# Kernel optimization log

Measured on AMD Instinct MI355X. Metric: run time of the kernel, lower is better.

The kernel has to match this reference:

```python
import jax, jax.numpy as jnp
import numpy as np

IN_FEATURES = 4096
OUT_FEATURES = 11008
GROUP_SIZE = 128


def setup_inputs() -> dict:
    key = jax.random.key(0)
    k_x, k_w, k_s, k_z, k_b = jax.random.split(key, 5)
    x = jax.random.normal(k_x, (8, IN_FEATURES), dtype=jnp.float32)
    # packed INT4 weights: two 4-bit values per byte, stored in int32 (0..255)
    weight_q = jax.random.randint(k_w, (OUT_FEATURES, IN_FEATURES // 2), 0, 256, dtype=jnp.int32)
    num_groups = IN_FEATURES // GROUP_SIZE  # 32
    scales = jax.random.uniform(k_s, (OUT_FEATURES, num_groups), dtype=jnp.float32) * 0.01 + 1e-4
    zeros = jax.random.normal(k_z, (OUT_FEATURES, num_groups), dtype=jnp.float32) * 0.05
    bias = jax.random.normal(k_b, (OUT_FEATURES,), dtype=jnp.float32) * 0.02
    return {"x": x, "weight_q": weight_q, "scales": scales, "zeros": zeros, "bias": bias}


def _dequantize(weight_q, scales, zeros):
    # unpack INT4: low nibble first, then high nibble (matches torch stack order)
    low = weight_q & 15
    high = (weight_q >> 4) & 15
    q = jnp.stack([low, high], axis=-1).reshape(OUT_FEATURES, -1)  # [out, in]
    q = q.astype(scales.dtype)
    num_groups = scales.shape[1]
    q = q[:, : num_groups * GROUP_SIZE].reshape(OUT_FEATURES, num_groups, GROUP_SIZE)
    w = q * scales[:, :, None] + zeros[:, :, None]
    return w.reshape(OUT_FEATURES, -1)[:, :IN_FEATURES]


def reference(x, weight_q, scales, zeros, bias):
    w = _dequantize(weight_q, scales, zeros)            # [out, in]
    return x.astype(w.dtype) @ w.T + bias               # [B, out]
```

## Files before the change

kernel.cpp:

```cpp
#include <hip/hip_runtime.h>

typedef _Float16 f16;
typedef __attribute__((ext_vector_type(2))) _Float16 f16x2;
typedef __attribute__((ext_vector_type(8))) _Float16 f16x8;
typedef __attribute__((ext_vector_type(4))) float f32x4;
typedef __attribute__((ext_vector_type(4))) unsigned u32x4;

constexpr int IN_F  = 4096;
constexpr int OUT_F = 11008;
constexpr int NGRP  = 32;

__device__ __forceinline__ unsigned dq2(unsigned q, f16x2 sp, f16x2 zp) {
    unsigned t = (((q << 12) | q) & 0x000F000Fu) | 0x64006400u;
    f16x2 u = __builtin_bit_cast(f16x2, t);
    u = u - (f16x2){(_Float16)1024.0f, (_Float16)1024.0f};
    u = u * sp + zp;
    return __builtin_bit_cast(unsigned, u);
}

__device__ __forceinline__ f16x2 bcast(float v) {
    _Float16 h = (_Float16)v;
    return (f16x2){h, h};
}

__global__ __launch_bounds__(256, 4)
void qlin_kernel(const int* __restrict__ wq,
                 const float* __restrict__ scales,
                 const float* __restrict__ zeros,
                 const float* __restrict__ bias,
                 const float* __restrict__ xf,
                 float* __restrict__ out)
{
    __shared__ unsigned char wlds[2][16][1024];
    __shared__ f32x4 red[4][64];

    const int tid  = threadIdx.x;
    const int wv   = tid >> 6;
    const int lane = tid & 63;
    const int col  = lane & 15;
    const int kg   = lane >> 4;
    const int o0   = blockIdx.x * 16;
    const int orow = o0 + col;
    const bool mvalid = (col < 8);

    f16x2 sp[8], zp[8];
    #pragma unroll
    for (int s = 0; s < 8; ++s) {
        sp[s] = bcast(scales[(size_t)orow * NGRP + s * 4 + wv]);
        zp[s] = bcast(zeros [(size_t)orow * NGRP + s * 4 + wv]);
    }

    const char* wtile = (const char*)wq + (size_t)o0 * 8192;

    auto stage = [&](int sl, int bufi) {
        #pragma unroll
        for (int c = 0; c < 4; ++c) {
            const int r = 4 * wv + c;
            const char* src = wtile + (size_t)r * 8192 + sl * 1024
                              + ((lane * 16) ^ ((r & 7) << 4));
            __builtin_amdgcn_global_load_lds(
                (const __attribute__((address_space(1))) void*)src,
                (__attribute__((address_space(3))) void*)&wlds[bufi][r][0],
                16, 0, 0);
        }
    };

    stage(0, 0);
    stage(1, 1);

    const float* xfcol = xf + (size_t)col * IN_F;
    const unsigned swz = (unsigned)((col & 7) << 4);

    f32x4 acc = {0.f, 0.f, 0.f, 0.f};

    #pragma unroll
    for (int s = 0; s < 8; ++s) {
        if (s < 7) asm volatile("s_waitcnt vmcnt(4)" ::: "memory");
        else       asm volatile("s_waitcnt vmcnt(0)" ::: "memory");
        __builtin_amdgcn_s_barrier();
        asm volatile("" ::: "memory");

        const f16x2 s2 = sp[s], z2 = zp[s];
        #pragma unroll
        for (int t = 0; t < 4; ++t) {
            const int k = s * 512 + wv * 128 + t * 32 + kg * 8;
            f16x8 af = (f16x8){0,0,0,0,0,0,0,0};
            if (mvalid) {
                float4 a0 = *(const float4*)(xfcol + k);
                float4 a1 = *(const float4*)(xfcol + k + 4);
                af = (f16x8){(f16)a0.x,(f16)a0.y,(f16)a0.z,(f16)a0.w,
                             (f16)a1.x,(f16)a1.y,(f16)a1.z,(f16)a1.w};
            }
            const unsigned off = ((unsigned)(wv * 256 + t * 64 + kg * 16)) ^ swz;
            const int4 q = *(const int4*)&wlds[s & 1][col][off];
            u32x4 bw = {dq2((unsigned)q.x, s2, z2),
                        dq2((unsigned)q.y, s2, z2),
                        dq2((unsigned)q.z, s2, z2),
                        dq2((unsigned)q.w, s2, z2)};
            f16x8 bfr = __builtin_bit_cast(f16x8, bw);
            acc = __builtin_amdgcn_mfma_f32_16x16x32_f16(af, bfr, acc, 0, 0, 0);
        }

        asm volatile("" ::: "memory");
        __builtin_amdgcn_s_barrier();
        if (s < 6) stage(s + 2, s & 1);
    }

    red[wv][lane] = acc;
    __syncthreads();

    if (tid < 64) {
        f32x4 ssum = red[0][tid];
        #pragma unroll
        for (int w = 1; w < 4; ++w) ssum += red[w][tid];
        const int n = tid & 15;
        const float bb = bias[o0 + n];
        const int mbase = (tid >> 4) * 4;
        if (mbase < 8) {
            #pragma unroll
            for (int i = 0; i < 4; ++i)
                out[(size_t)(mbase + i) * OUT_F + o0 + n] = ssum[i] + bb;
        }
    }
}

extern "C" void kernel_launch(void* const* d_in, const int* in_sizes, int n_in,
                              void* d_out, int out_size, void* d_ws, size_t ws_size,
                              hipStream_t stream) {
    const float* x  = (const float*)d_in[0];
    const int*   wq = (const int*)d_in[1];
    const float* sc = (const float*)d_in[2];
    const float* zr = (const float*)d_in[3];
    const float* bs = (const float*)d_in[4];
    float* out = (float*)d_out;
    (void)d_ws; (void)ws_size; (void)in_sizes; (void)n_in;

    qlin_kernel<<<OUT_F / 16, 256, 0, stream>>>(wq, sc, zr, bs, x, out);
}
```

Baseline: 31.70 us.

## Split K across four blocks with workspace partials and a separate reduce kernel

New measurement: 27.67 us. 12.7% less time.

```diff
diff --git a/kernel.cpp b/kernel.cpp
--- a/kernel.cpp
+++ b/kernel.cpp
@@ -9,6 +9,8 @@
 constexpr int IN_F  = 4096;
 constexpr int OUT_F = 11008;
 constexpr int NGRP  = 32;
+constexpr int NTILE = OUT_F / 16;
+constexpr int PLANE = OUT_F * 8;
 
 __device__ __forceinline__ unsigned dq2(unsigned q, f16x2 sp, f16x2 zp) {
     unsigned t = (((q << 12) | q) & 0x000F000Fu) | 0x64006400u;
@@ -21,6 +23,115 @@
 __device__ __forceinline__ f16x2 bcast(float v) {
     _Float16 h = (_Float16)v;
     return (f16x2){h, h};
+}
+
+__global__ __launch_bounds__(256, 4)
+void qlin_partial(const int* __restrict__ wq,
+                  const float* __restrict__ scales,
+                  const float* __restrict__ zeros,
+                  const float* __restrict__ xf,
+                  float* __restrict__ wsf)
+{
+    __shared__ unsigned char wlds[4][8192];
+    __shared__ f32x4 red[4][64];
+
+    const int tid  = threadIdx.x;
+    const int wv   = tid >> 6;
+    const int lane = tid & 63;
+    const int col  = lane & 15;
+    const int kg   = lane >> 4;
+    const int bid  = blockIdx.x;
+    const int kq   = bid & 3;
+    const int ot   = bid >> 2;
+    const int o0   = ot * 16;
+    const int orow = o0 + col;
+    const bool mvalid = (col < 8);
+
+    const int k0 = kq * 1024 + wv * 256;
+    const int g0 = k0 >> 7;
+
+    const f16x2 sp0 = bcast(scales[(size_t)orow * NGRP + g0]);
+    const f16x2 sp1 = bcast(scales[(size_t)orow * NGRP + g0 + 1]);
+    const f16x2 zp0 = bcast(zeros [(size_t)orow * NGRP + g0]);
+    const f16x2 zp1 = bcast(zeros [(size_t)orow * NGRP + g0 + 1]);
+
+    const char* wb = (const char*)wq;
+    #pragma unroll
+    for (int c = 0; c < 8; ++c) {
+        const int r    = 2 * c + (lane >> 5);
+        const size_t grow = (size_t)(o0 + r);
+        const char* src = wb + grow * 8192 + (size_t)k0 * 2
+                          + (((lane & 31) * 16) ^ ((r & 7) << 4));
+        __builtin_amdgcn_global_load_lds(
+            (const __attribute__((address_space(1))) void*)src,
+            (__attribute__((address_space(3))) void*)&wlds[wv][c * 1024],
+            16, 0, 0);
+    }
+
+    float4 xr[16];
+    if (mvalid) {
+        const float* xp = xf + (size_t)col * IN_F + k0 + kg * 8;
+        #pragma unroll
+        for (int t = 0; t < 8; ++t) {
+            xr[2 * t]     = *(const float4*)(xp + t * 32);
+            xr[2 * t + 1] = *(const float4*)(xp + t * 32 + 4);
+        }
+    } else {
+        #pragma unroll
+        for (int i = 0; i < 16; ++i) xr[i] = (float4){0.f, 0.f, 0.f, 0.f};
+    }
+
+    asm volatile("s_waitcnt vmcnt(0)" ::: "memory");
+    __builtin_amdgcn_sched_barrier(0);
+
+    const unsigned swz = (unsigned)((col & 7) << 4);
+    const unsigned base = (unsigned)(wv * 8192 + col * 512);
+    const unsigned char* lf = &wlds[0][0];
+
+    f32x4 acc = {0.f, 0.f, 0.f, 0.f};
+    #pragma unroll
+    for (int t = 0; t < 8; ++t) {
+        f16x8 af = (f16x8){(f16)xr[2*t].x,   (f16)xr[2*t].y,   (f16)xr[2*t].z,   (f16)xr[2*t].w,
+                           (f16)xr[2*t+1].x, (f16)xr[2*t+1].y, (f16)xr[2*t+1].z, (f16)xr[2*t+1].w};
+        const unsigned off = base + (((unsigned)(t * 64 + kg * 16)) ^ swz);
+        const int4 q = *(const int4*)(lf + off);
+        const f16x2 s2 = (t < 4) ? sp0 : sp1;
+        const f16x2 z2 = (t < 4) ? zp0 : zp1;
+        u32x4 bw = {dq2((unsigned)q.x, s2, z2),
+                    dq2((unsigned)q.y, s2, z2),
+                    dq2((unsigned)q.z, s2, z2),
+                    dq2((unsigned)q.w, s2, z2)};
+        f16x8 bfr = __builtin_bit_cast(f16x8, bw);
+        acc = __builtin_amdgcn_mfma_f32_16x16x32_f16(af, bfr, acc, 0, 0, 0);
+    }
+
+    red[wv][lane] = acc;
+    __syncthreads();
+
+    if (tid < 64) {
+        f32x4 ssum = red[0][tid];
+        #pragma unroll
+        for (int w = 1; w < 4; ++w) ssum += red[w][tid];
+        const int n = tid & 15;
+        const int mbase = (tid >> 4) * 4;
+        if (mbase < 8) {
+            float* plane = wsf + (size_t)kq * PLANE;
+            #pragma unroll
+            for (int i = 0; i < 4; ++i)
+                plane[(size_t)(mbase + i) * OUT_F + o0 + n] = ssum[i];
+        }
+    }
+}
+
+__global__ __launch_bounds__(256)
+void reduce_kernel(const float* __restrict__ wsf,
+                   const float* __restrict__ bias,
+                   float* __restrict__ out)
+{
+    const int idx = blockIdx.x * 256 + threadIdx.x;
+    const int o = idx % OUT_F;
+    out[idx] = bias[o] + wsf[idx] + wsf[PLANE + idx]
+             + wsf[2 * PLANE + idx] + wsf[3 * PLANE + idx];
 }
 
 __global__ __launch_bounds__(256, 4)
@@ -51,7 +162,6 @@
     }
 
     const char* wtile = (const char*)wq + (size_t)o0 * 8192;
-
     auto stage = [&](int sl, int bufi) {
         #pragma unroll
         for (int c = 0; c < 4; ++c) {
@@ -70,13 +180,11 @@
 
     const float* xfcol = xf + (size_t)col * IN_F;
     const unsigned swz = (unsigned)((col & 7) << 4);
-
     f32x4 acc = {0.f, 0.f, 0.f, 0.f};
 
     #pragma unroll
     for (int s = 0; s < 8; ++s) {
-        if (s < 7) asm volatile("s_waitcnt vmcnt(4)" ::: "memory");
-        else       asm volatile("s_waitcnt vmcnt(0)" ::: "memory");
+        asm volatile("s_waitcnt vmcnt(0)" ::: "memory");
         __builtin_amdgcn_s_barrier();
         asm volatile("" ::: "memory");
 
@@ -133,7 +241,13 @@
     const float* zr = (const float*)d_in[3];
     const float* bs = (const float*)d_in[4];
     float* out = (float*)d_out;
-    (void)d_ws; (void)ws_size; (void)in_sizes; (void)n_in;
-
-    qlin_kernel<<<OUT_F / 16, 256, 0, stream>>>(wq, sc, zr, bs, x, out);
-}
+    (void)in_sizes; (void)n_in;
+
+    if (ws_size >= (size_t)4 * PLANE * sizeof(float)) {
+        float* wsf = (float*)d_ws;
+        qlin_partial<<<NTILE * 4, 256, 0, stream>>>(wq, sc, zr, x, wsf);
+        reduce_kernel<<<PLANE / 256, 256, 0, stream>>>(wsf, bs, out);
+    } else {
+        qlin_kernel<<<NTILE, 256, 0, stream>>>(wq, sc, zr, bs, x, out);
+    }
+}
```
